# Performance work log

Hardware: AMD Instinct MI355X
Metric: run time of the kernel (lower is better)

## Reference

```python
import jax, jax.numpy as jnp
import numpy as np


def setup_inputs() -> dict:
    key = jax.random.key(0)
    k1, k2, k3 = jax.random.split(key, 3)
    inp = jax.random.normal(k1, (32, 128, 56, 56), dtype=jnp.float32)
    # kaiming-style scale for a 3x3 conv kernel
    fan_in = 128 * 3 * 3
    kernel = jax.random.normal(k2, (256, 128, 3, 3), dtype=jnp.float32) * np.float32(np.sqrt(2.0 / fan_in))
    bias = jax.random.normal(k3, (256,), dtype=jnp.float32)
    return {"inp": inp, "kernel": kernel, "bias": bias}


def reference(inp, kernel, bias):
    # 3x3 conv, stride 1, padding 1 (SAME), NCHW / OIHW layout, plus bias.
    out = jax.lax.conv_general_dilated(
        inp, kernel,
        window_strides=(1, 1),
        padding=((1, 1), (1, 1)),
        dimension_numbers=("NCHW", "OIHW", "NCHW"),
    )
    return out + bias[None, :, None, None]
```

## Files before the change

### kernel.cpp

```cpp
#include <hip/hip_runtime.h>
#include <hip/hip_bf16.h>


#define C_IN   128
#define K_OUT  256
#define HW     56
#define IMG    3136
#define NBATCH 32
#define PW     58
#define PLANE  3364
#define PADTOT (16*NBATCH*PLANE*8)
#define KTOT   1152

typedef __bf16 bf16x8 __attribute__((ext_vector_type(8)));
typedef float  f32x4  __attribute__((ext_vector_type(4)));
typedef unsigned short ushort8 __attribute__((ext_vector_type(8)));

__device__ inline unsigned short f2bf(float f) {
    unsigned int u = __builtin_bit_cast(unsigned int, f);
    u += ((u >> 16) & 1u) + 0x7FFFu;
    return (unsigned short)(u >> 16);
}

__device__ __forceinline__ void gl2lds16(const unsigned short* g, unsigned short* l) {
    __builtin_amdgcn_global_load_lds(
        (const __attribute__((address_space(1))) unsigned int*)g,
        (__attribute__((address_space(3))) unsigned int*)l, 16, 0, 0);
}

__global__ void prep_input(const float* __restrict__ inp,
                           unsigned short* __restrict__ dst) {
    __shared__ unsigned short tile[C_IN * 57];
    int n = blockIdx.x / PW, py = blockIdx.x % PW;
    ushort8* d8 = (ushort8*)dst;
    const bool border = (py == 0 || py == PW - 1);
    if (!border) {
        const float* src = inp + (size_t)n * C_IN * IMG + (py - 1) * HW;
        for (int i = threadIdx.x; i < C_IN * HW; i += 256) {
            int c = i / HW, x = i - c * HW;
            tile[c * 57 + x] = f2bf(src[c * IMG + x]);
        }
        __syncthreads();
    }
    for (int i = threadIdx.x; i < 16 * PW; i += 256) {
        int seg = i / PW, X = i - seg * PW;
        ushort8 v = (ushort8)0;
        if (!border && X >= 1 && X <= HW) {
#pragma unroll
            for (int e = 0; e < 8; ++e) v[e] = tile[(seg * 8 + e) * 57 + (X - 1)];
        }
        d8[((seg * NBATCH + n) * PW + py) * PW + X] = v;
    }
}

__global__ void prep_weights(const float* __restrict__ w,
                             unsigned short* __restrict__ dst) {
    int idx = blockIdx.x * 256 + threadIdx.x;
    int chunk = idx >> 3, e = idx & 7;
    int p = chunk / 3072, rem = chunk - p * 3072;
    int s = rem >> 10, rem2 = rem & 1023;
    int cc = rem2 >> 8, ko = rem2 & 255;
    int cq = p / 3, r = p - 3 * cq;
    int c = cq * 32 + cc * 8 + e;
    dst[idx] = f2bf(w[(ko * C_IN + c) * 9 + r * 3 + s]);
}

__global__ __launch_bounds__(512, 2) void conv_mfma(
        const unsigned short* __restrict__ In,
        const unsigned short* __restrict__ Wt,
        const float* __restrict__ bias,
        float* __restrict__ out) {
    __shared__ unsigned short smem[73728];

    const int tid = threadIdx.x;
    const int lane = tid & 63, wv = tid >> 6;
    const int l15 = lane & 15, lk = lane >> 4;
    const int blk = blockIdx.x;
    const int n = blk / 14, rb = (blk % 14) * 4;
    const int nb = n * PLANE + rb * PW;

    const int wko = (wv & 3) * 64;
    const int wpx = (wv >> 2) * 112;
    const int albase = lk * 4096 + (wko + l15) * 16;

    int rowoff[7];
#pragma unroll
    for (int nf = 0; nf < 7; ++nf) {
        int p = wpx + nf * 16 + l15;
        int yl = p / 56, x = p - yl * 56;
        rowoff[nf] = lk * 5568 + (yl * 58 + x) * 16;
    }

    f32x4 acc[4][7];
#pragma unroll
    for (int m = 0; m < 4; ++m)
#pragma unroll
        for (int nf = 0; nf < 7; ++nf) acc[m][nf] = (f32x4)0.0f;

#define STAGE_W(PHN) do {                                                   \
    _Pragma("unroll")                                                       \
    for (int li = 0; li < 6; ++li) {                                        \
        int chunk = li * 512 + tid;                                         \
        gl2lds16(Wt + (PHN) * 24576 + chunk * 8,                            \
                 &smem[((PHN) & 1) * 24576 + chunk * 8]);                   \
    } } while (0)

#define STAGE_I(CQN, R_) do {                                               \
    int chunk = (R_) * 512 + tid;                                           \
    int ch2 = chunk < 1392 ? chunk : 0;                                     \
    int cc_ = ch2 / 348, rem_ = ch2 - cc_ * 348;                            \
    gl2lds16(In + (((CQN) * 4 + cc_) * (NBATCH * PLANE) + nb + rem_) * 8,   \
             &smem[49152 + ((CQN) & 1) * 12288 + chunk * 8]);               \
} while (0)

    STAGE_W(0);
    STAGE_I(0, 0); STAGE_I(0, 1); STAGE_I(0, 2);

#define PHASE(PH) do {                                                      \
    constexpr int cq_ = (PH) / 3, r_ = (PH) % 3;                            \
    if ((PH) < 11) { STAGE_W((PH) + 1); }                                   \
    if (cq_ < 3)   { STAGE_I(cq_ + 1, r_); }                                \
    asm volatile("s_waitcnt vmcnt(%0)"                                      \
                 :: "i"((PH) < 9 ? 7 : ((PH) < 11 ? 6 : 0)) : "memory");    \
    __builtin_amdgcn_s_barrier();                                           \
    { const char* wb = (const char*)smem + ((PH) & 1) * 49152;              \
      const char* ib = (const char*)smem + 98304 + (cq_ & 1) * 24576;       \
      __builtin_amdgcn_s_setprio(1);                                        \
      _Pragma("unroll")                                                     \
      for (int s = 0; s < 3; ++s) {                                         \
          bf16x8 a[4], b[7];                                                \
          _Pragma("unroll")                                                 \
          for (int m = 0; m < 4; ++m)                                       \
              a[m] = *(const bf16x8*)(wb + albase + s * 16384 + m * 256);   \
          _Pragma("unroll")                                                 \
          for (int nf = 0; nf < 7; ++nf)                                    \
              b[nf] = *(const bf16x8*)(ib + rowoff[nf] + (r_ * 58 + s) * 16); \
          _Pragma("unroll")                                                 \
          for (int m = 0; m < 4; ++m)                                       \
              _Pragma("unroll")                                             \
              for (int nf = 0; nf < 7; ++nf)                                \
                  acc[m][nf] = __builtin_amdgcn_mfma_f32_16x16x32_bf16(     \
                      a[m], b[nf], acc[m][nf], 0, 0, 0);                    \
      }                                                                     \
      __builtin_amdgcn_s_setprio(0);                                        \
    }                                                                       \
    __builtin_amdgcn_s_barrier();                                           \
} while (0)

    PHASE(0);  PHASE(1);  PHASE(2);  PHASE(3);
    PHASE(4);  PHASE(5);  PHASE(6);  PHASE(7);
    PHASE(8);  PHASE(9);  PHASE(10); PHASE(11);

#undef PHASE
#undef STAGE_I
#undef STAGE_W

    const int sp0 = rb * 56 + wpx;
#pragma unroll
    for (int m = 0; m < 4; ++m) {
        int kb = wko + m * 16 + lk * 4;
        f32x4 bs = *(const f32x4*)(bias + kb);
#pragma unroll
        for (int nf = 0; nf < 7; ++nf) {
            float* ob = out + ((size_t)(n * K_OUT + kb) * IMG) + sp0 + nf * 16 + l15;
#pragma unroll
            for (int j = 0; j < 4; ++j)
                ob[(size_t)j * IMG] = acc[m][nf][j] + bs[j];
        }
    }
}

__global__ void conv_naive(const float* __restrict__ inp,
                           const float* __restrict__ ker,
                           const float* __restrict__ bias,
                           float* __restrict__ out, int total) {
    int o = blockIdx.x * blockDim.x + threadIdx.x;
    if (o >= total) return;
    int x = o % HW, y = (o / HW) % HW, ko = (o / IMG) % K_OUT, n = o / (IMG * K_OUT);
    float acc = bias[ko];
    for (int c = 0; c < C_IN; ++c)
        for (int r = 0; r < 3; ++r) {
            int iy = y + r - 1; if ((unsigned)iy >= HW) continue;
            for (int s = 0; s < 3; ++s) {
                int ix = x + s - 1; if ((unsigned)ix >= HW) continue;
                acc += inp[((n * C_IN + c) * HW + iy) * HW + ix]
                     * ker[((ko * C_IN + c) * 3 + r) * 3 + s];
            }
        }
    out[o] = acc;
}

extern "C" void kernel_launch(void* const* d_in, const int* in_sizes, int n_in,
                              void* d_out, int out_size, void* d_ws, size_t ws_size,
                              hipStream_t stream) {
    const float* inp  = (const float*)d_in[0];
    const float* ker  = (const float*)d_in[1];
    const float* bias = (const float*)d_in[2];
    float* out = (float*)d_out;

    const size_t need = (size_t)PADTOT * 2 + (size_t)K_OUT * KTOT * 2;
    if (ws_size < need) {
        int total = NBATCH * K_OUT * IMG;
        conv_naive<<<(total + 255) / 256, 256, 0, stream>>>(inp, ker, bias, out, total);
        return;
    }

    unsigned short* inb = (unsigned short*)d_ws;
    unsigned short* wtb = inb + (size_t)PADTOT;

    prep_input<<<NBATCH * PW, 256, 0, stream>>>(inp, inb);
    prep_weights<<<(K_OUT * KTOT) / 256, 256, 0, stream>>>(ker, wtb);

    conv_mfma<<<448, 512, 0, stream>>>(inb, wtb, bias, out);
}
```

Before: 85.54 us.

## Rearrange bf16 input and weight layouts for bank-conflict-free LDS fragment reads

Input and weight workspaces now use a new layout that interleaves the 4 channel sub-groups (cc) with 16-pixel or 16-output-channel groups, so each MFMA fragment read by a wavefront covers a contiguous 1 KB region. Input rows are padded to 256 chunks of 64 columns, which makes the input staging a simple contiguous copy without the chunk clamp and division. B-operand addresses are precomputed per kernel column offset s. The aim is to remove LDS bank conflicts and cut address arithmetic, at the cost of a slightly larger padded input buffer and more address registers.

```diff
diff --git a/kernel.cpp b/kernel.cpp
--- a/kernel.cpp
+++ b/kernel.cpp
@@ -8,9 +8,9 @@
 #define IMG    3136
 #define NBATCH 32
 #define PW     58
-#define PLANE  3364
-#define PADTOT (16*NBATCH*PLANE*8)
 #define KTOT   1152
+#define IN_WS_USHORT ((size_t)4*NBATCH*PW*256*8)
+#define WT_WS_USHORT ((size_t)12*3072*8)
 
 typedef __bf16 bf16x8 __attribute__((ext_vector_type(8)));
 typedef float  f32x4  __attribute__((ext_vector_type(4)));
@@ -42,14 +42,17 @@
         }
         __syncthreads();
     }
-    for (int i = threadIdx.x; i < 16 * PW; i += 256) {
-        int seg = i / PW, X = i - seg * PW;
+    for (int i = threadIdx.x; i < 1024; i += 256) {
+        int cq = i >> 8, rem = i & 255;
+        int X = ((rem >> 6) & 3) * 16 + (rem & 15);
+        int cc = (rem >> 4) & 3;
         ushort8 v = (ushort8)0;
         if (!border && X >= 1 && X <= HW) {
 #pragma unroll
-            for (int e = 0; e < 8; ++e) v[e] = tile[(seg * 8 + e) * 57 + (X - 1)];
-        }
-        d8[((seg * NBATCH + n) * PW + py) * PW + X] = v;
+            for (int e = 0; e < 8; ++e)
+                v[e] = tile[(cq * 32 + cc * 8 + e) * 57 + (X - 1)];
+        }
+        d8[((size_t)(cq * NBATCH + n) * PW + py) * 256 + rem] = v;
     }
 }
 
@@ -59,7 +62,8 @@
     int chunk = idx >> 3, e = idx & 7;
     int p = chunk / 3072, rem = chunk - p * 3072;
     int s = rem >> 10, rem2 = rem & 1023;
-    int cc = rem2 >> 8, ko = rem2 & 255;
+    int koq = rem2 >> 6, cc = (rem2 >> 4) & 3, kor = rem2 & 15;
+    int ko = koq * 16 + kor;
     int cq = p / 3, r = p - 3 * cq;
     int c = cq * 32 + cc * 8 + e;
     dst[idx] = f2bf(w[(ko * C_IN + c) * 9 + r * 3 + s]);
@@ -77,18 +81,21 @@
     const int l15 = lane & 15, lk = lane >> 4;
     const int blk = blockIdx.x;
     const int n = blk / 14, rb = (blk % 14) * 4;
-    const int nb = n * PLANE + rb * PW;
 
     const int wko = (wv & 3) * 64;
     const int wpx = (wv >> 2) * 112;
-    const int albase = lk * 4096 + (wko + l15) * 16;
-
-    int rowoff[7];
+    const int albase = (wv & 3) * 4096 + lk * 256 + l15 * 16;
+
+    int addrB[3][7];
 #pragma unroll
     for (int nf = 0; nf < 7; ++nf) {
         int p = wpx + nf * 16 + l15;
         int yl = p / 56, x = p - yl * 56;
-        rowoff[nf] = lk * 5568 + (yl * 58 + x) * 16;
+#pragma unroll
+        for (int s = 0; s < 3; ++s) {
+            int X = x + s;
+            addrB[s][nf] = yl * 4096 + (X >> 4) * 1024 + lk * 256 + (X & 15) * 16;
+        }
     }
 
     f32x4 acc[4][7];
@@ -107,9 +114,7 @@
 
 #define STAGE_I(CQN, R_) do {                                               \
     int chunk = (R_) * 512 + tid;                                           \
-    int ch2 = chunk < 1392 ? chunk : 0;                                     \
-    int cc_ = ch2 / 348, rem_ = ch2 - cc_ * 348;                            \
-    gl2lds16(In + (((CQN) * 4 + cc_) * (NBATCH * PLANE) + nb + rem_) * 8,   \
+    gl2lds16(In + ((size_t)((CQN) * NBATCH + n) * PW + rb) * 2048 + chunk * 8, \
              &smem[49152 + ((CQN) & 1) * 12288 + chunk * 8]);               \
 } while (0)
 
@@ -131,10 +136,10 @@
           bf16x8 a[4], b[7];                                                \
           _Pragma("unroll")                                                 \
           for (int m = 0; m < 4; ++m)                                       \
-              a[m] = *(const bf16x8*)(wb + albase + s * 16384 + m * 256);   \
+              a[m] = *(const bf16x8*)(wb + albase + s * 16384 + m * 1024);  \
           _Pragma("unroll")                                                 \
           for (int nf = 0; nf < 7; ++nf)                                    \
-              b[nf] = *(const bf16x8*)(ib + rowoff[nf] + (r_ * 58 + s) * 16); \
+              b[nf] = *(const bf16x8*)(ib + addrB[s][nf] + r_ * 4096);      \
           _Pragma("unroll")                                                 \
           for (int m = 0; m < 4; ++m)                                       \
               _Pragma("unroll")                                             \
@@ -198,7 +203,7 @@
     const float* bias = (const float*)d_in[2];
     float* out = (float*)d_out;
 
-    const size_t need = (size_t)PADTOT * 2 + (size_t)K_OUT * KTOT * 2;
+    const size_t need = (IN_WS_USHORT + WT_WS_USHORT) * 2;
     if (ws_size < need) {
         int total = NBATCH * K_OUT * IMG;
         conv_naive<<<(total + 255) / 256, 256, 0, stream>>>(inp, ker, bias, out, total);
@@ -206,7 +211,7 @@
     }
 
     unsigned short* inb = (unsigned short*)d_ws;
-    unsigned short* wtb = inb + (size_t)PADTOT;
+    unsigned short* wtb = inb + IN_WS_USHORT;
 
     prep_input<<<NBATCH * PW, 256, 0, stream>>>(inp, inb);
     prep_weights<<<(K_OUT * KTOT) / 256, 256, 0, stream>>>(ker, wtb);
```

Measured after the change: 83.53 us. 1.02x faster.
